# Kernel tuning notes

Measured on AMD Instinct MI355X. Metric: run time of the kernel, lower is better.

The kernel has to match this reference:

```python
import jax, jax.numpy as jnp
from jax import lax
import numpy as np

N = 4096      # graph nodes
K = 16        # sampled local-neighborhood size (2-hop proxy)
T = 16        # number of templates
NT = 16       # nodes per template
D = 128       # node feature dim
OUTER = 3     # proximal / mirror-descent iterations
INNER = 5     # sinkhorn iterations per outer step
EPS_REL = 0.1 # entropic reg relative to cost range
TINY = 1e-16


def setup_inputs() -> dict:
    key = jax.random.key(0)
    ks = jax.random.split(key, 8)
    x = jax.random.normal(ks[0], (N, D), jnp.float32)
    adj = (jax.random.uniform(ks[1], (N, N)) < 0.004).astype(jnp.float32)
    adj = jnp.maximum(adj, adj.T)
    neighbors = jax.random.randint(ks[2], (N, K), 0, N, dtype=jnp.int32)
    templates = (jax.random.randint(ks[3], (T, NT, NT), 0, 2).astype(jnp.float32)
                 + 0.01 * jax.random.normal(ks[4], (T, NT, NT), jnp.float32))
    templates_features = 0.0012 + 0.02 * jax.random.normal(ks[5], (T, NT, D), jnp.float32)
    q0 = jax.random.uniform(ks[6], (T, NT), jnp.float32)
    alpha0 = jnp.zeros((1,), jnp.float32)
    return {"x": x, "adj": adj, "neighbors": neighbors, "templates": templates,
            "templates_features": templates_features, "q0": q0, "alpha0": alpha0}


def _ltfgw(x, adj, neighbors, templates, templates_features, q0, alpha0):
    n, d = x.shape
    t, nt, _ = templates.shape
    k1 = neighbors.shape[1] + 1
    nb = jnp.concatenate([jnp.arange(n, dtype=neighbors.dtype)[:, None], neighbors], axis=1)  # [N,K1]
    Fi = x[nb]                                    # [N,K1,D] local node features
    C1 = adj[nb[:, :, None], nb[:, None, :]]      # [N,K1,K1] local structure
    C2 = templates                                # [T,NT,NT]
    alpha = jax.nn.sigmoid(alpha0[0])
    q = jax.nn.softmax(q0, axis=1)                # [T,NT] template node weights
    p = jnp.full((k1,), 1.0 / k1, x.dtype)        # uniform local weights
    # squared-euclidean feature cost M: [N,T,K1,NT]
    M = (jnp.sum(Fi**2, -1)[:, None, :, None]
         + jnp.sum(templates_features**2, -1)[None, :, None, :]
         - 2.0 * jnp.einsum('nkd,tmd->ntkm', Fi, templates_features))
    # constant part of squared-loss GW cost
    cC = (jnp.einsum('nij,j->ni', C1**2, p)[:, None, :, None]
          + jnp.einsum('tm,tlm->tl', q, C2**2)[None, :, None, :])
    G0 = jnp.broadcast_to(p[None, None, :, None] * q[None, :, None, :], (n, t, k1, nt))

    def outer_step(G, _):
        gw_grad = cC - 2.0 * jnp.einsum('nij,ntjm,tlm->ntil', C1, G, C2)
        grad = (1.0 - alpha) * M + alpha * gw_grad
        lo = jnp.min(grad, axis=(-2, -1), keepdims=True)
        hi = jnp.max(grad, axis=(-2, -1), keepdims=True)
        eps = EPS_REL * (hi - lo) + TINY
        Kmat = jnp.exp(-(grad - lo) / eps)        # per-(n,t) shift leaves plan invariant

        def sink(uv, _):
            u, v = uv
            u = p[None, None, :] / jnp.maximum(jnp.einsum('ntkm,ntm->ntk', Kmat, v), TINY)
            v = q[None] / jnp.maximum(jnp.einsum('ntkm,ntk->ntm', Kmat, u), TINY)
            return (u, v), None

        u0 = jnp.ones((n, t, k1), x.dtype)
        v0 = jnp.ones((n, t, nt), x.dtype)
        (u, v), _ = lax.scan(sink, (u0, v0), None, length=INNER)
        return u[..., None] * Kmat * v[..., None, :], None

    G, _ = lax.scan(outer_step, G0, None, length=OUTER)
    gw = cC - 2.0 * jnp.einsum('nij,ntjm,tlm->ntil', C1, G, C2)
    # fused GW distance of every node's local graph to every template: [N,T]
    return jnp.sum(((1.0 - alpha) * M + alpha * gw) * G, axis=(-2, -1))


def reference(x, adj, neighbors, templates, templates_features, q0, alpha0):
    return _ltfgw(x, adj, neighbors, templates, templates_features, q0, alpha0)
```

## Files before the change

### kernel.cpp

```cpp
#include <hip/hip_runtime.h>
#include <math.h>


#define NN 4096
#define KNB 16
#define K1 17
#define C1STRIDE 20
#define C1NODE 340
#define TSTR 296
#define TINYF 1e-16f

typedef const __attribute__((address_space(4))) float* c4fp;
typedef const __attribute__((address_space(4))) int*   c4ip;
__device__ __forceinline__ float sload(const float* p){ return *(c4fp)(unsigned long long)p; }
__device__ __forceinline__ int   sloadi(const int* p) { return *(c4ip)(unsigned long long)p; }

template<int CTRL>
__device__ __forceinline__ float dppmov(float x) {
  return __int_as_float(
      __builtin_amdgcn_update_dpp(0, __float_as_int(x), CTRL, 0xF, 0xF, true));
}
__device__ __forceinline__ float xor4v(float x) {
  return dppmov<0x1B>(dppmov<0x141>(x));
}
__device__ __forceinline__ float rsum16(float x) {
  x += dppmov<0xB1>(x); x += dppmov<0x4E>(x);
  x += xor4v(x);        x += dppmov<0x128>(x);
  return x;
}
__device__ __forceinline__ float rmin16(float x) {
  x = fminf(x, dppmov<0xB1>(x)); x = fminf(x, dppmov<0x4E>(x));
  x = fminf(x, xor4v(x));        x = fminf(x, dppmov<0x128>(x));
  return x;
}
__device__ __forceinline__ float rmax16(float x) {
  x = fmaxf(x, dppmov<0xB1>(x)); x = fmaxf(x, dppmov<0x4E>(x));
  x = fmaxf(x, xor4v(x));        x = fmaxf(x, dppmov<0x128>(x));
  return x;
}
__device__ __forceinline__ float rcpn(float x) {
  float r = __builtin_amdgcn_rcpf(x);
  return r * (2.f - x * r);
}

#define WSTEP(C, R) { g = dppmov<C>(g); acc = fmaf(g, c2reg[R], acc); }
#define WALK15() \
  WSTEP(0xB1,1)  WSTEP(0x1B,2)  WSTEP(0xB1,3)  WSTEP(0x141,4) \
  WSTEP(0xB1,5)  WSTEP(0x1B,6)  WSTEP(0xB1,7)  WSTEP(0x140,8) \
  WSTEP(0xB1,9)  WSTEP(0x1B,10) WSTEP(0xB1,11) WSTEP(0x141,12) \
  WSTEP(0xB1,13) WSTEP(0x1B,14) WSTEP(0xB1,15)

#define PG_GEMM  256
#define PG_PACK  (PG_GEMM + 1024)
#define PG_XSQ   (PG_PACK + 1024)
#define PG_SCAL  PG_XSQ
#define PG_TOT   (PG_SCAL + 1)

__global__ __launch_bounds__(256) void prep_combined(
    const float* __restrict__ x, const float* __restrict__ adj,
    const float* __restrict__ templates_, const float* __restrict__ tf,
    const float* __restrict__ q0, const float* __restrict__ alpha0,
    float* __restrict__ P, unsigned long long* __restrict__ pk,
    float* __restrict__ xsq, float* __restrict__ tfsq,
    float* __restrict__ qmat, float* __restrict__ cq,
    float* __restrict__ walpha) {
  __shared__ __align__(16) float smem[2 * 64 * 68];
  const int b = blockIdx.x, tid = threadIdx.x;

  if (b < PG_GEMM) {
    float (*As)[68] = (float (*)[68])smem;
    float (*Bs)[68] = (float (*)[68])(smem + 64 * 68);
    int tx = tid & 15, ty = tid >> 4;
    int r0 = (b & 63) * 64, c0 = (b >> 6) * 64;
    float acc[4][4] = {};
    for (int h = 0; h < 2; ++h) {
      __syncthreads();
#pragma unroll
      for (int q = 0; q < 4; ++q) {
        int f = tid + 256*q;
        int row = f >> 4, d4 = (f & 15) << 2;
        float4 a = *(const float4*)&x[(r0+row)*128 + h*64 + d4];
        As[d4+0][row]=a.x; As[d4+1][row]=a.y; As[d4+2][row]=a.z; As[d4+3][row]=a.w;
        float4 bb = *(const float4*)&tf[(c0+row)*128 + h*64 + d4];
        Bs[d4+0][row]=bb.x; Bs[d4+1][row]=bb.y; Bs[d4+2][row]=bb.z; Bs[d4+3][row]=bb.w;
      }
      __syncthreads();
#pragma unroll
      for (int d = 0; d < 64; ++d) {
        float4 a = *(const float4*)&As[d][ty*4];
        float4 bb = *(const float4*)&Bs[d][tx*4];
        float av[4]={a.x,a.y,a.z,a.w}, bv[4]={bb.x,bb.y,bb.z,bb.w};
#pragma unroll
        for (int i = 0; i < 4; ++i)
#pragma unroll
          for (int j = 0; j < 4; ++j) acc[i][j] = fmaf(av[i], bv[j], acc[i][j]);
      }
    }
#pragma unroll
    for (int i = 0; i < 4; ++i) {
      float4 o; o.x=acc[i][0]; o.y=acc[i][1]; o.z=acc[i][2]; o.w=acc[i][3];
      *(float4*)&P[(r0 + ty*4 + i)*256 + c0 + tx*4] = o;
    }
    return;
  }

  if (b < PG_PACK) {
    int wave = (b - PG_GEMM)*4 + (tid >> 6);
    int lane = tid & 63;
#pragma unroll 4
    for (int it = 0; it < 64; ++it) {
      int w64 = wave + it*4096;
      float v = adj[(size_t)w64*64 + lane];
      unsigned long long m = __ballot(v != 0.f);
      if (lane == 0) pk[w64] = m;
    }
    return;
  }

  if (b < PG_XSQ) {
    int n = (b - PG_PACK)*4 + (tid >> 6), lane = tid & 63;
    float2 v = *(const float2*)&x[n*128 + lane*2];
    float s = fmaf(v.x, v.x, v.y*v.y);
    s += __shfl_xor(s,1); s += __shfl_xor(s,2);  s += __shfl_xor(s,4);
    s += __shfl_xor(s,8); s += __shfl_xor(s,16); s += __shfl_xor(s,32);
    if (lane == 0) xsq[n] = s;
    return;
  }

  {
    int t = tid >> 4, l = tid & 15;
    if (tid == 0) walpha[0] = 1.f / (1.f + expf(-alpha0[0]));
    float qr[16]; float mx = -3.0e38f;
#pragma unroll
    for (int m = 0; m < 16; ++m) { qr[m] = q0[t*16+m]; mx = fmaxf(mx, qr[m]); }
    float s = 0.f;
#pragma unroll
    for (int m = 0; m < 16; ++m) { qr[m] = expf(qr[m]-mx); s += qr[m]; }
    float inv = 1.f / s;
    qmat[tid] = qr[l] * inv;
    float c = 0.f;
#pragma unroll
    for (int m = 0; m < 16; ++m) {
      float c2 = templates_[t*256 + l*16 + m];
      c = fmaf(qr[m]*inv, c2*c2, c);
    }
    cq[tid] = c;
    float ts = 0.f;
#pragma unroll
    for (int dq = 0; dq < 32; ++dq) {
      float4 v = *(const float4*)&tf[tid*128 + dq*4];
      ts = fmaf(v.x,v.x,ts); ts = fmaf(v.y,v.y,ts);
      ts = fmaf(v.z,v.z,ts); ts = fmaf(v.w,v.w,ts);
    }
    tfsq[tid] = ts;
  }
}

__global__ __launch_bounds__(256) void c1gather_packed(
    const unsigned* __restrict__ pku, const int* __restrict__ neighbors,
    float* __restrict__ C1ws) {
  __shared__ int nbs[K1];
  __shared__ float c1sh[K1 * K1];
  int n = blockIdx.x;
  int tid = threadIdx.x;
  if (tid < K1) nbs[tid] = (tid == 0) ? n : neighbors[n*KNB + tid - 1];
  __syncthreads();
  for (int e = tid; e < 289; e += 256) {
    int i = e / 17, j = e % 17;
    int col = nbs[j];
    unsigned w = pku[nbs[i]*128 + (col >> 5)];
    float v = ((w >> (col & 31)) & 1u) ? 1.f : 0.f;
    C1ws[n*C1NODE + i*C1STRIDE + j] = v;
    c1sh[e] = v;
  }
  __syncthreads();
  bool nz = false;
  if (tid < K1) {
    float s = 0.f;
#pragma unroll
    for (int j = 0; j < K1; ++j) {
      float v = c1sh[tid*17 + j];
      s = fmaf(v, v, s); nz |= (v != 0.f);
    }
    C1ws[n*C1NODE + tid*C1STRIDE + 17] = s * (1.f/17.f);
  }
  unsigned long long bal = __ballot(nz);
  if (tid == 0)
    ((int*)C1ws)[n*C1NODE + 18] = (int)(bal & 0x1FFFF);
}

__global__ __launch_bounds__(256, 2) void ltfgw_main(
    const float* __restrict__ P, const float* __restrict__ C1ws,
    const float* __restrict__ xsq, const float* __restrict__ tfsq,
    const float* __restrict__ qmat, const float* __restrict__ cq,
    const float* __restrict__ walpha, const int* __restrict__ neighbors,
    const float* __restrict__ templates_, float* __restrict__ out) {
  __shared__ __align__(16) float Ksh[16 * TSTR];
  __shared__ __align__(16) float Ush[256];
  __shared__ __align__(16) float Vsh[256];

  const int tid = threadIdx.x;
  const int t = tid >> 4, l = tid & 15;
  const int n = blockIdx.x;

  const float alpha = sload(walpha);
  const float oma = 1.f - alpha;
  const float na2 = -2.f * alpha;
  const int mask = sloadi((const int*)C1ws + n*C1NODE + 18);

  int nbk[K1];
  nbk[0] = n;
#pragma unroll
  for (int k = 1; k < K1; ++k) nbk[k] = sloadi(neighbors + n*KNB + (k-1));

  const float tfsq_l = tfsq[tid];
  const float cq_l   = cq[tid];
  const float q_l    = qmat[tid];

  float Mcol[K1];
#pragma unroll
  for (int k = 0; k < K1; ++k) {
    float xs  = sload(xsq + nbk[k]);
    float cc1 = sload(C1ws + n*C1NODE + k*C1STRIDE + 17);
    float pv  = P[nbk[k]*256 + tid];
    Mcol[k] = oma * (xs + tfsq_l - 2.f*pv) + alpha * (cc1 + cq_l);
  }

  float c2reg[16];
#pragma unroll
  for (int r = 0; r < 16; ++r)
    c2reg[r] = na2 * templates_[t*256 + l*16 + (l ^ r)];

  float Gcol[K1];
#pragma unroll
  for (int j = 0; j < K1; ++j) Gcol[j] = (1.f/17.f) * q_l;

  const int tb = t * TSTR;
  float ur[16], u16 = 0.f, vm = 1.f;

#pragma unroll 1
  for (int outer = 0; outer < 3; ++outer) {
    float Kc[K1];
    float lo = 3.0e38f, hi = -3.0e38f;
#pragma unroll
    for (int i = 0; i < K1; ++i) {
      float gr = Mcol[i];
      if (mask & (1 << i)) {
        const float* c1r = C1ws + n*C1NODE + i*C1STRIDE;
        float s = 0.f;
#pragma unroll
        for (int j = 0; j < K1; ++j) s = fmaf(sload(c1r + j), Gcol[j], s);
        float g = s, acc = s * c2reg[0];
        WALK15()
        gr += acc;
      }
      Kc[i] = gr;
      lo = fminf(lo, gr); hi = fmaxf(hi, gr);
    }
    lo = rmin16(lo); hi = rmax16(hi);
    float eps = 0.1f * (hi - lo) + TINYF;
    float sc = 1.4426950408889634f * __builtin_amdgcn_rcpf(eps);
#pragma unroll
    for (int i = 0; i < K1; ++i) {
      Kc[i] = __builtin_amdgcn_exp2f((lo - Kc[i]) * sc);
      Ksh[tb + i*17 + l] = Kc[i];
    }
    float Krow[16];
#pragma unroll
    for (int jq = 0; jq < 4; ++jq) {
      float4 v = *(const float4*)&Ksh[tb + l*17 + jq*4];
      Krow[jq*4+0]=v.x; Krow[jq*4+1]=v.y; Krow[jq*4+2]=v.z; Krow[jq*4+3]=v.w;
    }

    float vlane = 1.f;
    Vsh[tid] = 1.f;
#pragma unroll 1
    for (int it = 0; it < 5; ++it) {
      float vr[16];
#pragma unroll
      for (int q = 0; q < 4; ++q) {
        float4 v = *(const float4*)&Vsh[t*16 + q*4];
        vr[q*4+0]=v.x; vr[q*4+1]=v.y; vr[q*4+2]=v.z; vr[q*4+3]=v.w;
      }
      float w = 0.f;
#pragma unroll
      for (int j = 0; j < 16; ++j) w = fmaf(Krow[j], vr[j], w);
      float w16 = rsum16(Kc[16] * vlane);
      float um = (1.f/17.f) * rcpn(fmaxf(w,   TINYF));
      u16      = (1.f/17.f) * rcpn(fmaxf(w16, TINYF));
      Ush[tid] = um;
#pragma unroll
      for (int q = 0; q < 4; ++q) {
        float4 v = *(const float4*)&Ush[t*16 + q*4];
        ur[q*4+0]=v.x; ur[q*4+1]=v.y; ur[q*4+2]=v.z; ur[q*4+3]=v.w;
      }
      float sg = u16 * Kc[16];
#pragma unroll
      for (int k = 0; k < 16; ++k) sg = fmaf(ur[k], Kc[k], sg);
      vlane = q_l * rcpn(fmaxf(sg, TINYF));
      Vsh[tid] = vlane;
    }
    vm = vlane;
#pragma unroll
    for (int k = 0; k < 16; ++k) Gcol[k] = ur[k] * Kc[k] * vm;
    Gcol[16] = u16 * Kc[16] * vm;
  }

  float acc1 = 0.f;
#pragma unroll
  for (int i = 0; i < K1; ++i) acc1 = fmaf(Mcol[i], Gcol[i], acc1);
#pragma unroll
  for (int i = 0; i < K1; ++i) {
    if (mask & (1 << i)) {
      const float* c1r = C1ws + n*C1NODE + i*C1STRIDE;
      float s = 0.f;
#pragma unroll
      for (int j = 0; j < K1; ++j) s = fmaf(sload(c1r + j), Gcol[j], s);
      float g = s, acc = s * c2reg[0];
      WALK15()
      acc1 = fmaf(acc, Gcol[i], acc1);
    }
  }
  float accout = rsum16(acc1);
  if (l == 0) out[n*16 + t] = accout;
}

extern "C" void kernel_launch(void* const* d_in, const int* in_sizes, int n_in,
                              void* d_out, int out_size, void* d_ws, size_t ws_size,
                              hipStream_t stream) {
  const float* x          = (const float*)d_in[0];
  const float* adj        = (const float*)d_in[1];
  const int*   neighbors  = (const int*)  d_in[2];
  const float* templates_ = (const float*)d_in[3];
  const float* tfeat      = (const float*)d_in[4];
  const float* q0         = (const float*)d_in[5];
  const float* alpha0     = (const float*)d_in[6];
  float* out = (float*)d_out;

  float* ws     = (float*)d_ws;
  float* P      = ws;
  float* C1ws   = P + 4096*256;
  float* xsq    = C1ws + 4096*C1NODE;
  float* tfsq   = xsq + 4096;
  float* qmat   = tfsq + 256;
  float* cq     = qmat + 256;
  float* walpha = cq + 256;
  unsigned long long* pk = (unsigned long long*)(walpha + 8);

  hipLaunchKernelGGL(prep_combined, dim3(PG_TOT), dim3(256), 0, stream,
                     x, adj, templates_, tfeat, q0, alpha0,
                     P, pk, xsq, tfsq, qmat, cq, walpha);
  hipLaunchKernelGGL(c1gather_packed, dim3(4096), dim3(256), 0, stream,
                     (const unsigned*)pk, neighbors, C1ws);
  hipLaunchKernelGGL(ltfgw_main, dim3(4096), dim3(256), 0, stream,
                     P, C1ws, xsq, tfsq, qmat, cq, walpha, neighbors,
                     templates_, out);
}
```

Before: 198.7 us.

## Fuse C1 gather into main kernel as per-row bitmasks, retile feature GEMM

Drops the separate c1gather kernel and its dense float C1 workspace. Each main block now builds 17 row bitmasks from the packed adjacency in shared memory and derives the C1-squared row sums with popcount. The C1·G products become masked additions selected by wave-uniform bits instead of scalar loads of float entries. The prep GEMM tile shrinks to 32x64 so twice as many blocks run. This saves one launch and the workspace traffic, but adds a gather and a barrier at the start of the main kernel.

```diff
diff --git a/kernel.cpp b/kernel.cpp
--- a/kernel.cpp
+++ b/kernel.cpp
@@ -5,8 +5,6 @@
 #define NN 4096
 #define KNB 16
 #define K1 17
-#define C1STRIDE 20
-#define C1NODE 340
 #define TSTR 296
 #define TINYF 1e-16f
 
@@ -50,7 +48,7 @@
   WSTEP(0xB1,9)  WSTEP(0x1B,10) WSTEP(0xB1,11) WSTEP(0x141,12) \
   WSTEP(0xB1,13) WSTEP(0x1B,14) WSTEP(0xB1,15)
 
-#define PG_GEMM  256
+#define PG_GEMM  512
 #define PG_PACK  (PG_GEMM + 1024)
 #define PG_XSQ   (PG_PACK + 1024)
 #define PG_SCAL  PG_XSQ
@@ -69,37 +67,42 @@
 
   if (b < PG_GEMM) {
     float (*As)[68] = (float (*)[68])smem;
-    float (*Bs)[68] = (float (*)[68])(smem + 64 * 68);
+    float (*Bs)[68] = (float (*)[68])(smem + 64*68);
     int tx = tid & 15, ty = tid >> 4;
-    int r0 = (b & 63) * 64, c0 = (b >> 6) * 64;
-    float acc[4][4] = {};
+    int r0 = (b & 127) * 32, c0 = (b >> 7) * 64;
+    float acc[2][4] = {};
     for (int h = 0; h < 2; ++h) {
       __syncthreads();
 #pragma unroll
-      for (int q = 0; q < 4; ++q) {
+      for (int q = 0; q < 2; ++q) {
         int f = tid + 256*q;
         int row = f >> 4, d4 = (f & 15) << 2;
         float4 a = *(const float4*)&x[(r0+row)*128 + h*64 + d4];
         As[d4+0][row]=a.x; As[d4+1][row]=a.y; As[d4+2][row]=a.z; As[d4+3][row]=a.w;
-        float4 bb = *(const float4*)&tf[(c0+row)*128 + h*64 + d4];
-        Bs[d4+0][row]=bb.x; Bs[d4+1][row]=bb.y; Bs[d4+2][row]=bb.z; Bs[d4+3][row]=bb.w;
+      }
+#pragma unroll
+      for (int q = 0; q < 4; ++q) {
+        int f = tid + 256*q;
+        int col = f >> 4, d4 = (f & 15) << 2;
+        float4 bb = *(const float4*)&tf[(c0+col)*128 + h*64 + d4];
+        Bs[d4+0][col]=bb.x; Bs[d4+1][col]=bb.y; Bs[d4+2][col]=bb.z; Bs[d4+3][col]=bb.w;
       }
       __syncthreads();
 #pragma unroll
       for (int d = 0; d < 64; ++d) {
-        float4 a = *(const float4*)&As[d][ty*4];
+        float2 a = *(const float2*)&As[d][ty*2];
         float4 bb = *(const float4*)&Bs[d][tx*4];
-        float av[4]={a.x,a.y,a.z,a.w}, bv[4]={bb.x,bb.y,bb.z,bb.w};
-#pragma unroll
-        for (int i = 0; i < 4; ++i)
+        float av[2]={a.x,a.y}, bv[4]={bb.x,bb.y,bb.z,bb.w};
+#pragma unroll
+        for (int i = 0; i < 2; ++i)
 #pragma unroll
           for (int j = 0; j < 4; ++j) acc[i][j] = fmaf(av[i], bv[j], acc[i][j]);
       }
     }
 #pragma unroll
-    for (int i = 0; i < 4; ++i) {
+    for (int i = 0; i < 2; ++i) {
       float4 o; o.x=acc[i][0]; o.y=acc[i][1]; o.z=acc[i][2]; o.w=acc[i][3];
-      *(float4*)&P[(r0 + ty*4 + i)*256 + c0 + tx*4] = o;
+      *(float4*)&P[(r0 + ty*2 + i)*256 + c0 + tx*4] = o;
     }
     return;
   }
@@ -156,41 +159,8 @@
   }
 }
 
-__global__ __launch_bounds__(256) void c1gather_packed(
-    const unsigned* __restrict__ pku, const int* __restrict__ neighbors,
-    float* __restrict__ C1ws) {
-  __shared__ int nbs[K1];
-  __shared__ float c1sh[K1 * K1];
-  int n = blockIdx.x;
-  int tid = threadIdx.x;
-  if (tid < K1) nbs[tid] = (tid == 0) ? n : neighbors[n*KNB + tid - 1];
-  __syncthreads();
-  for (int e = tid; e < 289; e += 256) {
-    int i = e / 17, j = e % 17;
-    int col = nbs[j];
-    unsigned w = pku[nbs[i]*128 + (col >> 5)];
-    float v = ((w >> (col & 31)) & 1u) ? 1.f : 0.f;
-    C1ws[n*C1NODE + i*C1STRIDE + j] = v;
-    c1sh[e] = v;
-  }
-  __syncthreads();
-  bool nz = false;
-  if (tid < K1) {
-    float s = 0.f;
-#pragma unroll
-    for (int j = 0; j < K1; ++j) {
-      float v = c1sh[tid*17 + j];
-      s = fmaf(v, v, s); nz |= (v != 0.f);
-    }
-    C1ws[n*C1NODE + tid*C1STRIDE + 17] = s * (1.f/17.f);
-  }
-  unsigned long long bal = __ballot(nz);
-  if (tid == 0)
-    ((int*)C1ws)[n*C1NODE + 18] = (int)(bal & 0x1FFFF);
-}
-
 __global__ __launch_bounds__(256, 2) void ltfgw_main(
-    const float* __restrict__ P, const float* __restrict__ C1ws,
+    const float* __restrict__ P, const unsigned* __restrict__ pku,
     const float* __restrict__ xsq, const float* __restrict__ tfsq,
     const float* __restrict__ qmat, const float* __restrict__ cq,
     const float* __restrict__ walpha, const int* __restrict__ neighbors,
@@ -198,6 +168,7 @@
   __shared__ __align__(16) float Ksh[16 * TSTR];
   __shared__ __align__(16) float Ush[256];
   __shared__ __align__(16) float Vsh[256];
+  __shared__ int rowm[20];
 
   const int tid = threadIdx.x;
   const int t = tid >> 4, l = tid & 15;
@@ -206,12 +177,28 @@
   const float alpha = sload(walpha);
   const float oma = 1.f - alpha;
   const float na2 = -2.f * alpha;
-  const int mask = sloadi((const int*)C1ws + n*C1NODE + 18);
 
   int nbk[K1];
   nbk[0] = n;
 #pragma unroll
   for (int k = 1; k < K1; ++k) nbk[k] = sloadi(neighbors + n*KNB + (k-1));
+
+  if (tid < K1) {
+    int row = (tid == 0) ? n : neighbors[n*KNB + tid - 1];
+    const unsigned* prow = pku + row*128;
+    unsigned m = 0;
+#pragma unroll
+    for (int j = 0; j < K1; ++j) {
+      int col = nbk[j];
+      unsigned w = prow[col >> 5];
+      m |= ((w >> (col & 31)) & 1u) << j;
+    }
+    rowm[tid] = (int)m;
+  }
+  __syncthreads();
+  int rmv[K1];
+#pragma unroll
+  for (int i = 0; i < K1; ++i) rmv[i] = rowm[i];
 
   const float tfsq_l = tfsq[tid];
   const float cq_l   = cq[tid];
@@ -221,7 +208,7 @@
 #pragma unroll
   for (int k = 0; k < K1; ++k) {
     float xs  = sload(xsq + nbk[k]);
-    float cc1 = sload(C1ws + n*C1NODE + k*C1STRIDE + 17);
+    float cc1 = (float)__popc((unsigned)rmv[k]) * (1.f/17.f);
     float pv  = P[nbk[k]*256 + tid];
     Mcol[k] = oma * (xs + tfsq_l - 2.f*pv) + alpha * (cc1 + cq_l);
   }
@@ -245,11 +232,12 @@
 #pragma unroll
     for (int i = 0; i < K1; ++i) {
       float gr = Mcol[i];
-      if (mask & (1 << i)) {
-        const float* c1r = C1ws + n*C1NODE + i*C1STRIDE;
+      int rmi = __builtin_amdgcn_readfirstlane(rmv[i]);
+      if (rmi) {
         float s = 0.f;
 #pragma unroll
-        for (int j = 0; j < K1; ++j) s = fmaf(sload(c1r + j), Gcol[j], s);
+        for (int j = 0; j < K1; ++j)
+          if (rmi & (1 << j)) s += Gcol[j];
         float g = s, acc = s * c2reg[0];
         WALK15()
         gr += acc;
@@ -311,11 +299,12 @@
   for (int i = 0; i < K1; ++i) acc1 = fmaf(Mcol[i], Gcol[i], acc1);
 #pragma unroll
   for (int i = 0; i < K1; ++i) {
-    if (mask & (1 << i)) {
-      const float* c1r = C1ws + n*C1NODE + i*C1STRIDE;
+    int rmi = __builtin_amdgcn_readfirstlane(rmv[i]);
+    if (rmi) {
       float s = 0.f;
 #pragma unroll
-      for (int j = 0; j < K1; ++j) s = fmaf(sload(c1r + j), Gcol[j], s);
+      for (int j = 0; j < K1; ++j)
+        if (rmi & (1 << j)) s += Gcol[j];
       float g = s, acc = s * c2reg[0];
       WALK15()
       acc1 = fmaf(acc, Gcol[i], acc1);
@@ -339,8 +328,7 @@
 
   float* ws     = (float*)d_ws;
   float* P      = ws;
-  float* C1ws   = P + 4096*256;
-  float* xsq    = C1ws + 4096*C1NODE;
+  float* xsq    = P + 4096*256;
   float* tfsq   = xsq + 4096;
   float* qmat   = tfsq + 256;
   float* cq     = qmat + 256;
@@ -350,9 +338,7 @@
   hipLaunchKernelGGL(prep_combined, dim3(PG_TOT), dim3(256), 0, stream,
                      x, adj, templates_, tfeat, q0, alpha0,
                      P, pk, xsq, tfsq, qmat, cq, walpha);
-  hipLaunchKernelGGL(c1gather_packed, dim3(4096), dim3(256), 0, stream,
-                     (const unsigned*)pk, neighbors, C1ws);
   hipLaunchKernelGGL(ltfgw_main, dim3(4096), dim3(256), 0, stream,
-                     P, C1ws, xsq, tfsq, qmat, cq, walpha, neighbors,
-                     templates_, out);
-}
+                     P, (const unsigned*)pk, xsq, tfsq, qmat, cq, walpha,
+                     neighbors, templates_, out);
+}
```

New measurement: 195.4 us. No clear change (-1.6%).
